# Performance work log

Measured on AMD Instinct MI355X. Metric: run time of the kernel, lower is better.

## Reference

```python
import jax, jax.numpy as jnp
import numpy as np


def sine_encode_2d(pos, d):
    # pos: (..., 2) normalized relative positions in [-1, 1]; output (..., d)
    # standard sinusoidal encoding per coordinate, d/2 dims each (sin/cos pairs)
    d_half = d // 2
    n_freq = d_half // 2
    freqs = jnp.exp(-jnp.log(jnp.float32(10000.0)) * jnp.arange(n_freq, dtype=jnp.float32) / n_freq)
    parts = []
    for i in range(2):
        ang = pos[..., i:i + 1] * freqs  # (..., n_freq)
        parts.append(jnp.sin(ang))
        parts.append(jnp.cos(ang))
    return jnp.concatenate(parts, axis=-1)


def rpe_bias(W_rpe, t_q, f_q, t_k, f_k, N_t, N_f, d_rpe):
    dt_norm = jnp.arange(-(N_t - 1), N_t, dtype=jnp.float32) / max(N_t - 1, 1)
    df_norm = jnp.arange(-(N_f - 1), N_f, dtype=jnp.float32) / max(N_f - 1, 1)
    DT, DF = jnp.meshgrid(dt_norm, df_norm, indexing='ij')       # (2Nt-1, 2Nf-1)
    rel = jnp.stack([DT, DF], axis=-1)                            # (2Nt-1, 2Nf-1, 2)
    enc = sine_encode_2d(rel, d_rpe)                              # (2Nt-1, 2Nf-1, d_rpe)
    table = enc @ W_rpe.T                                         # (2Nt-1, 2Nf-1, h)
    n_df = 2 * N_f - 1
    flat = table.reshape(-1, table.shape[-1])                     # ((2Nt-1)*(2Nf-1), h)
    dt_idx = t_q[:, None] - t_k[None, :] + (N_t - 1)              # (Nq, Nk)
    df_idx = f_q[:, None] - f_k[None, :] + (N_f - 1)
    flat_idx = jnp.clip(dt_idx * n_df + df_idx, 0, flat.shape[0] - 1)
    bias = flat[flat_idx]                                         # (Nq, Nk, h)
    return jnp.transpose(bias, (2, 0, 1))                         # (h, Nq, Nk)


def setup_inputs() -> dict:
    key = jax.random.key(0)
    ks = jax.random.split(key, 12)
    B, N_t, N_f, d_model, n_heads, d_rpe = 8, 14, 72, 256, 8, 32
    N = N_t * N_f
    s = 1.0 / np.sqrt(d_model)
    return {
        'q_tokens': jax.random.normal(ks[0], (B, N, d_model), jnp.float32),
        'k_tokens': jax.random.normal(ks[1], (B, N, d_model), jnp.float32),
        'v_tokens': jax.random.normal(ks[2], (B, N, d_model), jnp.float32),
        't_q': jax.random.randint(ks[3], (N,), 0, N_t),
        'f_q': jax.random.randint(ks[4], (N,), 0, N_f),
        't_k': jax.random.randint(ks[5], (N,), 0, N_t),
        'f_k': jax.random.randint(ks[6], (N,), 0, N_f),
        'N_t': N_t,
        'N_f': N_f,
        'W_q': jax.random.normal(ks[7], (d_model, d_model), jnp.float32) * s,
        'W_k': jax.random.normal(ks[8], (d_model, d_model), jnp.float32) * s,
        'W_v': jax.random.normal(ks[9], (d_model, d_model), jnp.float32) * s,
        'W_o': jax.random.normal(ks[10], (d_model, d_model), jnp.float32) * s,
        'W_rpe': jax.random.normal(ks[11], (n_heads, d_rpe), jnp.float32) * (1.0 / np.sqrt(d_rpe)),
    }


def reference(q_tokens, k_tokens, v_tokens, t_q, f_q, t_k, f_k, N_t, N_f,
              W_q, W_k, W_v, W_o, W_rpe):
    B, N_q, d_model = q_tokens.shape
    N_k = k_tokens.shape[1]
    h = W_rpe.shape[0]
    d_rpe = W_rpe.shape[1]
    dk = d_model // h
    scale = jnp.float32(np.sqrt(dk))
    Q = (q_tokens @ W_q.T).reshape(B, N_q, h, dk)
    K = (k_tokens @ W_k.T).reshape(B, N_k, h, dk)
    V = (v_tokens @ W_v.T).reshape(B, N_k, h, dk)
    scores = jnp.einsum('bqhd,bkhd->bhqk', Q, K) / scale          # (B, h, Nq, Nk)
    bias = rpe_bias(W_rpe, t_q, f_q, t_k, f_k, N_t, N_f, d_rpe)   # (h, Nq, Nk)
    attn = jax.nn.softmax(scores + bias[None], axis=-1)
    out = jnp.einsum('bhqk,bkhd->bqhd', attn, V).reshape(B, N_q, d_model)
    return out @ W_o.T
```

## Files before the change

### kernel.cpp

```cpp
#include <hip/hip_runtime.h>

#define B_    8
#define N_    1008
#define D_    256
#define H_    8
#define DK_   32
#define DA_   64
#define L2E_  1.4426950408889634f

typedef _Float16 half8_t __attribute__((ext_vector_type(8)));
typedef _Float16 half4_t __attribute__((ext_vector_type(4)));
typedef float    f32x4   __attribute__((ext_vector_type(4)));

#if defined(__has_builtin)
#if __has_builtin(__builtin_amdgcn_exp2f)
#define EXP2(x) __builtin_amdgcn_exp2f(x)
#else
#define EXP2(x) exp2f(x)
#endif
#else
#define EXP2(x) exp2f(x)
#endif

__global__ __launch_bounds__(256, 4) void qkv_prep(
    const float* __restrict__ q_tok, const float* __restrict__ k_tok,
    const float* __restrict__ v_tok,
    const int* __restrict__ t_q, const int* __restrict__ f_q,
    const int* __restrict__ t_k, const int* __restrict__ f_k,
    const float* __restrict__ Wq, const float* __restrict__ Wk,
    const float* __restrict__ Wv, const float* __restrict__ W_rpe,
    _Float16* __restrict__ Qq, _Float16* __restrict__ Kq,
    _Float16* __restrict__ Uq, _Float16* __restrict__ Vr,
    _Float16* __restrict__ Vt)
{
    __shared__ __align__(16) _Float16 fw[8 * 4 * 64 * 8];
    const int tid = threadIdx.x;
    const int lane = tid & 63, w = tid >> 6, quad = lane >> 4, l15 = lane & 15;
    const int id = blockIdx.x;

    if (id < 756) {
        const int mtile = id / 12, rem = id % 12, z = rem >> 2, ntile = rem & 3;
        const int m0 = mtile * 128, n0 = ntile * 64;
        const float* A = (z == 0) ? q_tok : (z == 1) ? k_tok : v_tok;
        const float* W = (z == 0) ? Wq : (z == 1) ? Wk : Wv;

        const float* Ar0 = &A[(size_t)(m0 + w * 16 + l15) * D_];
        const float* Ar1 = Ar0 + (size_t)64 * D_;
        float4 a00 = *(const float4*)&Ar0[quad * 8];
        float4 a01 = *(const float4*)&Ar0[quad * 8 + 4];
        float4 a10 = *(const float4*)&Ar1[quad * 8];
        float4 a11 = *(const float4*)&Ar1[quad * 8 + 4];

#pragma unroll
        for (int p = 0; p < 8; p++) {
            int g = p * 256 + tid;
            int ch = g >> 8, rem2 = g & 255, nt = rem2 >> 6, L = rem2 & 63;
            const float* src = &W[(size_t)(n0 + nt * 16 + (L & 15)) * D_ + ch * 32 + ((L >> 4) & 3) * 8];
            float4 w0 = *(const float4*)src;
            float4 w1 = *(const float4*)(src + 4);
            half8_t hv = {(_Float16)w0.x, (_Float16)w0.y, (_Float16)w0.z, (_Float16)w0.w,
                          (_Float16)w1.x, (_Float16)w1.y, (_Float16)w1.z, (_Float16)w1.w};
            *(half8_t*)&fw[g * 8] = hv;
        }
        __syncthreads();

        f32x4 acc[2][4] = {};
#pragma unroll
        for (int ch = 0; ch < 8; ch++) {
            half8_t af0 = {(_Float16)a00.x, (_Float16)a00.y, (_Float16)a00.z, (_Float16)a00.w,
                           (_Float16)a01.x, (_Float16)a01.y, (_Float16)a01.z, (_Float16)a01.w};
            half8_t af1 = {(_Float16)a10.x, (_Float16)a10.y, (_Float16)a10.z, (_Float16)a10.w,
                           (_Float16)a11.x, (_Float16)a11.y, (_Float16)a11.z, (_Float16)a11.w};
            if (ch < 7) {
                a00 = *(const float4*)&Ar0[(ch + 1) * 32 + quad * 8];
                a01 = *(const float4*)&Ar0[(ch + 1) * 32 + quad * 8 + 4];
                a10 = *(const float4*)&Ar1[(ch + 1) * 32 + quad * 8];
                a11 = *(const float4*)&Ar1[(ch + 1) * 32 + quad * 8 + 4];
            }
#pragma unroll
            for (int nt = 0; nt < 4; nt++) {
                half8_t bf = *(const half8_t*)&fw[((ch * 4 + nt) * 64 + lane) * 8];
                acc[0][nt] = __builtin_amdgcn_mfma_f32_16x16x32_f16(af0, bf, acc[0][nt], 0, 0, 0);
                acc[1][nt] = __builtin_amdgcn_mfma_f32_16x16x32_f16(af1, bf, acc[1][nt], 0, 0, 0);
            }
        }
        const float scale = (z == 0) ? 0.17677669529663687f * L2E_ : 1.0f;
#pragma unroll
        for (int mt = 0; mt < 2; mt++) {
            int mbase = m0 + mt * 64 + w * 16 + quad * 4;
            int b = mbase / N_;
            int q = mbase - b * N_;
            if (z < 2) {
                _Float16* o = (z == 0) ? Qq : Kq;
#pragma unroll
                for (int nt = 0; nt < 4; nt++) {
                    int n = n0 + nt * 16 + l15;
                    int hh = n >> 5, d = n & 31;
                    _Float16* dst = &o[(((size_t)(b * 8 + hh)) * N_ + q) * DK_ + d];
#pragma unroll
                    for (int r = 0; r < 4; r++)
                        dst[(size_t)r * DK_] = (_Float16)(acc[mt][nt][r] * scale);
                }
            } else {
#pragma unroll
                for (int nt = 0; nt < 4; nt++) {
                    int n = n0 + nt * 16 + l15;
                    int hh = n >> 5, d = n & 31;
                    half4_t o = {(_Float16)acc[mt][nt][0], (_Float16)acc[mt][nt][1],
                                 (_Float16)acc[mt][nt][2], (_Float16)acc[mt][nt][3]};
                    *(half4_t*)&Vt[(((size_t)(b * 8 + hh)) * DK_ + d) * N_ + q] = o;
                }
            }
        }
    } else {
        const float FR[8] = {1.f, 0.31622776601683794f, 0.1f, 0.03162277660168379f,
                             0.01f, 0.0031622776601683794f, 0.001f, 0.00031622776601683794f};
        int gid = (id - 756) * 256 + tid;
        if (gid < N_ * H_) {
            int q = gid >> 3, h = gid & 7;
            float tq = (float)t_q[q] * (1.f / 13.f);
            float fq = (float)f_q[q] * (1.f / 71.f);
            const float* Wh = W_rpe + h * 32;
            half8_t u0, u1, u2, u3;
#pragma unroll
            for (int i = 0; i < 8; i++) {
                float sa = __sinf(tq * FR[i]), ca = __cosf(tq * FR[i]);
                float sb = __sinf(fq * FR[i]), cb = __cosf(fq * FR[i]);
                u0[i] = (_Float16)(L2E_ * (Wh[i] * sa + Wh[8 + i] * ca));
                u1[i] = (_Float16)(L2E_ * (Wh[8 + i] * sa - Wh[i] * ca));
                u2[i] = (_Float16)(L2E_ * (Wh[16 + i] * sb + Wh[24 + i] * cb));
                u3[i] = (_Float16)(L2E_ * (Wh[24 + i] * sb - Wh[16 + i] * cb));
            }
            _Float16* dst = &Uq[((size_t)h * N_ + q) * DK_];
            *(half8_t*)(dst + 0) = u0;  *(half8_t*)(dst + 8) = u1;
            *(half8_t*)(dst + 16) = u2; *(half8_t*)(dst + 24) = u3;
        } else if (gid < N_ * H_ + N_) {
            int k = gid - N_ * H_;
            float tk = (float)t_k[k] * (1.f / 13.f);
            float fk = (float)f_k[k] * (1.f / 71.f);
            half8_t v0, v1, v2, v3;
#pragma unroll
            for (int i = 0; i < 8; i++) {
                v0[i] = (_Float16)__cosf(tk * FR[i]);
                v1[i] = (_Float16)__sinf(tk * FR[i]);
                v2[i] = (_Float16)__cosf(fk * FR[i]);
                v3[i] = (_Float16)__sinf(fk * FR[i]);
            }
            _Float16* dst = &Vr[(size_t)k * DK_];
            *(half8_t*)(dst + 0) = v0;  *(half8_t*)(dst + 8) = v1;
            *(half8_t*)(dst + 16) = v2; *(half8_t*)(dst + 24) = v3;
        }
    }
}

__global__ __launch_bounds__(256, 4) void attn(const _Float16* __restrict__ Qq,
    const _Float16* __restrict__ Kq, const _Float16* __restrict__ Uq,
    const _Float16* __restrict__ Vr, const _Float16* __restrict__ Vt,
    _Float16* __restrict__ AO)
{
    __shared__ __align__(16) _Float16 fkl[2][4096];
    __shared__ __align__(16) _Float16 fvl[2][2048];
    __shared__ __align__(16) _Float16 pl[4][16][72];

    const int tid = threadIdx.x;
    const int lane = tid & 63, w = tid >> 6, quad = lane >> 4, l15 = lane & 15;
    const int bh = blockIdx.x, q0 = blockIdx.y * 64;
    const int b = bh >> 3, hh = bh & 7;
    const _Float16* Kb = Kq + (size_t)bh * N_ * DK_;
    const _Float16* Vb = Vt + (size_t)bh * DK_ * N_;

    const int s_l15 = tid & 15, s_quad = (tid >> 4) & 3;
    const int s_mt = tid >> 6;
    const int s_c = tid >> 7;
    const int s_mt2 = (tid >> 6) & 1;

    const int qg = q0 + w * 16 + l15;
    const int qc = qg < N_ ? qg : N_ - 1;
    half8_t qf0 = *(const half8_t*)&Qq[((size_t)bh * N_ + qc) * DK_ + quad * 8];
    half8_t qf1 = *(const half8_t*)&Uq[((size_t)hh * N_ + qc) * DK_ + quad * 8];

    float m_run = -1e30f, l_run = 0.f;
    f32x4 O[2] = {};

    {
        int krow = s_mt * 16 + s_l15;
        *(half8_t*)&fkl[0][((s_mt * 2 + 0) * 64 + lane) * 8] =
            *(const half8_t*)&Kb[(size_t)krow * DK_ + s_quad * 8];
        *(half8_t*)&fkl[0][((s_mt * 2 + 1) * 64 + lane) * 8] =
            *(const half8_t*)&Vr[(size_t)krow * DK_ + s_quad * 8];
        int vrow = s_mt2 * 16 + s_l15;
        int vcol = s_c * 32 + s_quad * 8;
        *(half8_t*)&fvl[0][tid * 8] = *(const half8_t*)&Vb[(size_t)vrow * N_ + vcol];
    }
    __syncthreads();

    for (int kt = 0; kt < 16; kt++) {
        const int cb = kt & 1;
        half8_t nk0, nk1, nv;
        if (kt < 15) {
            int k0n = (kt + 1) * 64;
            int krow = k0n + s_mt * 16 + s_l15;
            if (krow > N_ - 1) krow = N_ - 1;
            nk0 = *(const half8_t*)&Kb[(size_t)krow * DK_ + s_quad * 8];
            nk1 = *(const half8_t*)&Vr[(size_t)krow * DK_ + s_quad * 8];
            int vrow = s_mt2 * 16 + s_l15;
            int vcol = k0n + s_c * 32 + s_quad * 8;
            if (vcol > N_ - 8) vcol = N_ - 8;
            nv = *(const half8_t*)&Vb[(size_t)vrow * N_ + vcol];
        }
        f32x4 S[4];
        __builtin_amdgcn_s_setprio(1);
#pragma unroll
        for (int mt = 0; mt < 4; mt++) {
            half8_t kf0 = *(const half8_t*)&fkl[cb][((mt * 2 + 0) * 64 + lane) * 8];
            half8_t kf1 = *(const half8_t*)&fkl[cb][((mt * 2 + 1) * 64 + lane) * 8];
            f32x4 zz = {0.f, 0.f, 0.f, 0.f};
            zz = __builtin_amdgcn_mfma_f32_16x16x32_f16(kf0, qf0, zz, 0, 0, 0);
            S[mt] = __builtin_amdgcn_mfma_f32_16x16x32_f16(kf1, qf1, zz, 0, 0, 0);
        }
        __builtin_amdgcn_s_setprio(0);
        if (kt == 15)
            S[3] = (f32x4){-1e30f, -1e30f, -1e30f, -1e30f};
        float x0 = fmaxf(fmaxf(S[0][0], S[0][1]), fmaxf(S[0][2], S[0][3]));
        float x1 = fmaxf(fmaxf(S[1][0], S[1][1]), fmaxf(S[1][2], S[1][3]));
        float x2 = fmaxf(fmaxf(S[2][0], S[2][1]), fmaxf(S[2][2], S[2][3]));
        float x3 = fmaxf(fmaxf(S[3][0], S[3][1]), fmaxf(S[3][2], S[3][3]));
        float tmax = fmaxf(fmaxf(x0, x1), fmaxf(x2, x3));
        tmax = fmaxf(tmax, __shfl_xor(tmax, 16, 64));
        tmax = fmaxf(tmax, __shfl_xor(tmax, 32, 64));
        float mnew = fmaxf(m_run, tmax);
        float alpha = EXP2(m_run - mnew);
        m_run = mnew;
        float tsum = 0.f;
#pragma unroll
        for (int mt = 0; mt < 4; mt++) {
            float p0 = EXP2(S[mt][0] - mnew), p1 = EXP2(S[mt][1] - mnew);
            float p2 = EXP2(S[mt][2] - mnew), p3 = EXP2(S[mt][3] - mnew);
            tsum += (p0 + p1) + (p2 + p3);
            half4_t ph = {(_Float16)p0, (_Float16)p1, (_Float16)p2, (_Float16)p3};
            *(half4_t*)&pl[w][l15][mt * 16 + quad * 4] = ph;
        }
        tsum += __shfl_xor(tsum, 16, 64);
        tsum += __shfl_xor(tsum, 32, 64);
        l_run = l_run * alpha + tsum;
        O[0] = O[0] * alpha;
        O[1] = O[1] * alpha;
        __builtin_amdgcn_s_setprio(1);
#pragma unroll
        for (int c = 0; c < 2; c++) {
            half8_t pf = *(const half8_t*)&pl[w][l15][c * 32 + quad * 8];
            half8_t vfa = *(const half8_t*)&fvl[cb][((c * 2 + 0) * 64 + lane) * 8];
            half8_t vfb = *(const half8_t*)&fvl[cb][((c * 2 + 1) * 64 + lane) * 8];
            O[0] = __builtin_amdgcn_mfma_f32_16x16x32_f16(vfa, pf, O[0], 0, 0, 0);
            O[1] = __builtin_amdgcn_mfma_f32_16x16x32_f16(vfb, pf, O[1], 0, 0, 0);
        }
        __builtin_amdgcn_s_setprio(0);
        if (kt < 15) {
            *(half8_t*)&fkl[cb ^ 1][((s_mt * 2 + 0) * 64 + lane) * 8] = nk0;
            *(half8_t*)&fkl[cb ^ 1][((s_mt * 2 + 1) * 64 + lane) * 8] = nk1;
            *(half8_t*)&fvl[cb ^ 1][tid * 8] = nv;
        }
        __syncthreads();
    }
    if (qg < N_) {
        float inv = 1.f / l_run;
#pragma unroll
        for (int mt2 = 0; mt2 < 2; mt2++) {
            half4_t o = {(_Float16)(O[mt2][0] * inv), (_Float16)(O[mt2][1] * inv),
                         (_Float16)(O[mt2][2] * inv), (_Float16)(O[mt2][3] * inv)};
            *(half4_t*)&AO[((size_t)b * N_ + qg) * D_ + hh * DK_ + mt2 * 16 + quad * 4] = o;
        }
    }
}

__global__ __launch_bounds__(256, 4) void out_gemm(const _Float16* __restrict__ A,
    const float* __restrict__ W, float* __restrict__ out)
{
    __shared__ __align__(16) _Float16 fw[8 * 4 * 64 * 8];
    const int tid = threadIdx.x;
    const int lane = tid & 63, w = tid >> 6, quad = lane >> 4, l15 = lane & 15;
    const int id = blockIdx.x;
    const int m0 = (id >> 2) * 64, n0 = (id & 3) * 64;

    const _Float16* Ar = &A[(size_t)(m0 + w * 16 + l15) * D_];
    half8_t af = *(const half8_t*)&Ar[quad * 8];

#pragma unroll
    for (int p = 0; p < 8; p++) {
        int g = p * 256 + tid;
        int ch = g >> 8, rem2 = g & 255, nt = rem2 >> 6, L = rem2 & 63;
        const float* src = &W[(size_t)(n0 + nt * 16 + (L & 15)) * D_ + ch * 32 + ((L >> 4) & 3) * 8];
        float4 w0 = *(const float4*)src;
        float4 w1 = *(const float4*)(src + 4);
        half8_t hv = {(_Float16)w0.x, (_Float16)w0.y, (_Float16)w0.z, (_Float16)w0.w,
                      (_Float16)w1.x, (_Float16)w1.y, (_Float16)w1.z, (_Float16)w1.w};
        *(half8_t*)&fw[g * 8] = hv;
    }
    __syncthreads();

    f32x4 acc[4] = {};
#pragma unroll
    for (int ch = 0; ch < 8; ch++) {
        half8_t c0 = af;
        if (ch < 7) af = *(const half8_t*)&Ar[(ch + 1) * 32 + quad * 8];
#pragma unroll
        for (int nt = 0; nt < 4; nt++) {
            half8_t bf = *(const half8_t*)&fw[((ch * 4 + nt) * 64 + lane) * 8];
            acc[nt] = __builtin_amdgcn_mfma_f32_16x16x32_f16(c0, bf, acc[nt], 0, 0, 0);
        }
    }
    const int mbase = m0 + w * 16 + quad * 4;
#pragma unroll
    for (int nt = 0; nt < 4; nt++) {
        int n = n0 + nt * 16 + l15;
#pragma unroll
        for (int r = 0; r < 4; r++)
            out[(size_t)(mbase + r) * D_ + n] = acc[nt][r];
    }
}

extern "C" void kernel_launch(void* const* d_in, const int* in_sizes, int n_in,
                              void* d_out, int out_size, void* d_ws, size_t ws_size,
                              hipStream_t stream)
{
    const float* q_tokens = (const float*)d_in[0];
    const float* k_tokens = (const float*)d_in[1];
    const float* v_tokens = (const float*)d_in[2];
    const int*   t_q      = (const int*)d_in[3];
    const int*   f_q      = (const int*)d_in[4];
    const int*   t_k      = (const int*)d_in[5];
    const int*   f_k      = (const int*)d_in[6];
    const float* W_q   = (const float*)d_in[9];
    const float* W_k   = (const float*)d_in[10];
    const float* W_v   = (const float*)d_in[11];
    const float* W_o   = (const float*)d_in[12];
    const float* W_rpe = (const float*)d_in[13];

    _Float16* ws = (_Float16*)d_ws;
    _Float16* Qq = ws;
    _Float16* Kq = Qq + (size_t)64 * N_ * DK_;
    _Float16* Uq = Kq + (size_t)64 * N_ * DK_;
    _Float16* Vr = Uq + (size_t)H_ * N_ * DK_;
    _Float16* Vt = Vr + (size_t)N_ * DK_;
    _Float16* AO = Vt + (size_t)64 * DK_ * N_;

    qkv_prep<<<dim3(792), 256, 0, stream>>>(q_tokens, k_tokens, v_tokens,
                                            t_q, f_q, t_k, f_k,
                                            W_q, W_k, W_v, W_rpe,
                                            Qq, Kq, Uq, Vr, Vt);
    attn<<<dim3(64, 16), 256, 0, stream>>>(Qq, Kq, Uq, Vr, Vt, AO);
    out_gemm<<<dim3(504), 256, 0, stream>>>(AO, W_o, (float*)d_out);
}
```

Measured before the change: 145.8 us.

## Process two query tiles per attention block and skip small softmax rescales

Each attention workgroup now handles 128 queries instead of 64, with every wave carrying two 16-row query fragments. Each K/V tile staged in shared memory is therefore reused twice, and half as many blocks reload K and V. The online-softmax rescale is also skipped when the new tile max exceeds the running max by at most 8 (in log2 units) across the wavefront, which removes exp and multiply work but allows unnormalized probabilities up to 256 before fp16 conversion. Register pressure roughly doubles (launch bounds lowered to 2), and the grid shrinks to 512 blocks, which may reduce occupancy on the many-CU device.

```diff
diff --git a/kernel.cpp b/kernel.cpp
--- a/kernel.cpp
+++ b/kernel.cpp
@@ -153,18 +153,18 @@
     }
 }
 
-__global__ __launch_bounds__(256, 4) void attn(const _Float16* __restrict__ Qq,
+__global__ __launch_bounds__(256, 2) void attn(const _Float16* __restrict__ Qq,
     const _Float16* __restrict__ Kq, const _Float16* __restrict__ Uq,
     const _Float16* __restrict__ Vr, const _Float16* __restrict__ Vt,
     _Float16* __restrict__ AO)
 {
     __shared__ __align__(16) _Float16 fkl[2][4096];
     __shared__ __align__(16) _Float16 fvl[2][2048];
-    __shared__ __align__(16) _Float16 pl[4][16][72];
+    __shared__ __align__(16) _Float16 pl[4][2][16][72];
 
     const int tid = threadIdx.x;
     const int lane = tid & 63, w = tid >> 6, quad = lane >> 4, l15 = lane & 15;
-    const int bh = blockIdx.x, q0 = blockIdx.y * 64;
+    const int bh = blockIdx.x, q0 = blockIdx.y * 128;
     const int b = bh >> 3, hh = bh & 7;
     const _Float16* Kb = Kq + (size_t)bh * N_ * DK_;
     const _Float16* Vb = Vt + (size_t)bh * DK_ * N_;
@@ -174,13 +174,16 @@
     const int s_c = tid >> 7;
     const int s_mt2 = (tid >> 6) & 1;
 
-    const int qg = q0 + w * 16 + l15;
-    const int qc = qg < N_ ? qg : N_ - 1;
-    half8_t qf0 = *(const half8_t*)&Qq[((size_t)bh * N_ + qc) * DK_ + quad * 8];
-    half8_t qf1 = *(const half8_t*)&Uq[((size_t)hh * N_ + qc) * DK_ + quad * 8];
-
-    float m_run = -1e30f, l_run = 0.f;
-    f32x4 O[2] = {};
+    const int qgA = q0 + w * 16 + l15, qgB = qgA + 64;
+    const int qcA = qgA < N_ ? qgA : N_ - 1;
+    const int qcB = qgB < N_ ? qgB : N_ - 1;
+    half8_t qf0A = *(const half8_t*)&Qq[((size_t)bh * N_ + qcA) * DK_ + quad * 8];
+    half8_t qf1A = *(const half8_t*)&Uq[((size_t)hh * N_ + qcA) * DK_ + quad * 8];
+    half8_t qf0B = *(const half8_t*)&Qq[((size_t)bh * N_ + qcB) * DK_ + quad * 8];
+    half8_t qf1B = *(const half8_t*)&Uq[((size_t)hh * N_ + qcB) * DK_ + quad * 8];
+
+    float mA = -1e30f, lA = 0.f, mB = -1e30f, lB = 0.f;
+    f32x4 OA[2] = {}, OB[2] = {};
 
     {
         int krow = s_mt * 16 + s_l15;
@@ -208,51 +211,89 @@
             if (vcol > N_ - 8) vcol = N_ - 8;
             nv = *(const half8_t*)&Vb[(size_t)vrow * N_ + vcol];
         }
-        f32x4 S[4];
+        f32x4 SA[4], SB[4];
         __builtin_amdgcn_s_setprio(1);
 #pragma unroll
         for (int mt = 0; mt < 4; mt++) {
             half8_t kf0 = *(const half8_t*)&fkl[cb][((mt * 2 + 0) * 64 + lane) * 8];
             half8_t kf1 = *(const half8_t*)&fkl[cb][((mt * 2 + 1) * 64 + lane) * 8];
-            f32x4 zz = {0.f, 0.f, 0.f, 0.f};
-            zz = __builtin_amdgcn_mfma_f32_16x16x32_f16(kf0, qf0, zz, 0, 0, 0);
-            S[mt] = __builtin_amdgcn_mfma_f32_16x16x32_f16(kf1, qf1, zz, 0, 0, 0);
+            f32x4 za = {0.f, 0.f, 0.f, 0.f};
+            za = __builtin_amdgcn_mfma_f32_16x16x32_f16(kf0, qf0A, za, 0, 0, 0);
+            SA[mt] = __builtin_amdgcn_mfma_f32_16x16x32_f16(kf1, qf1A, za, 0, 0, 0);
+            f32x4 zb = {0.f, 0.f, 0.f, 0.f};
+            zb = __builtin_amdgcn_mfma_f32_16x16x32_f16(kf0, qf0B, zb, 0, 0, 0);
+            SB[mt] = __builtin_amdgcn_mfma_f32_16x16x32_f16(kf1, qf1B, zb, 0, 0, 0);
         }
         __builtin_amdgcn_s_setprio(0);
-        if (kt == 15)
-            S[3] = (f32x4){-1e30f, -1e30f, -1e30f, -1e30f};
-        float x0 = fmaxf(fmaxf(S[0][0], S[0][1]), fmaxf(S[0][2], S[0][3]));
-        float x1 = fmaxf(fmaxf(S[1][0], S[1][1]), fmaxf(S[1][2], S[1][3]));
-        float x2 = fmaxf(fmaxf(S[2][0], S[2][1]), fmaxf(S[2][2], S[2][3]));
-        float x3 = fmaxf(fmaxf(S[3][0], S[3][1]), fmaxf(S[3][2], S[3][3]));
-        float tmax = fmaxf(fmaxf(x0, x1), fmaxf(x2, x3));
-        tmax = fmaxf(tmax, __shfl_xor(tmax, 16, 64));
-        tmax = fmaxf(tmax, __shfl_xor(tmax, 32, 64));
-        float mnew = fmaxf(m_run, tmax);
-        float alpha = EXP2(m_run - mnew);
-        m_run = mnew;
-        float tsum = 0.f;
-#pragma unroll
-        for (int mt = 0; mt < 4; mt++) {
-            float p0 = EXP2(S[mt][0] - mnew), p1 = EXP2(S[mt][1] - mnew);
-            float p2 = EXP2(S[mt][2] - mnew), p3 = EXP2(S[mt][3] - mnew);
-            tsum += (p0 + p1) + (p2 + p3);
-            half4_t ph = {(_Float16)p0, (_Float16)p1, (_Float16)p2, (_Float16)p3};
-            *(half4_t*)&pl[w][l15][mt * 16 + quad * 4] = ph;
-        }
-        tsum += __shfl_xor(tsum, 16, 64);
-        tsum += __shfl_xor(tsum, 32, 64);
-        l_run = l_run * alpha + tsum;
-        O[0] = O[0] * alpha;
-        O[1] = O[1] * alpha;
+        if (kt == 15) {
+            SA[3] = (f32x4){-1e30f, -1e30f, -1e30f, -1e30f};
+            SB[3] = (f32x4){-1e30f, -1e30f, -1e30f, -1e30f};
+        }
+        {
+            float x0 = fmaxf(fmaxf(SA[0][0], SA[0][1]), fmaxf(SA[0][2], SA[0][3]));
+            float x1 = fmaxf(fmaxf(SA[1][0], SA[1][1]), fmaxf(SA[1][2], SA[1][3]));
+            float x2 = fmaxf(fmaxf(SA[2][0], SA[2][1]), fmaxf(SA[2][2], SA[2][3]));
+            float x3 = fmaxf(fmaxf(SA[3][0], SA[3][1]), fmaxf(SA[3][2], SA[3][3]));
+            float tmax = fmaxf(fmaxf(x0, x1), fmaxf(x2, x3));
+            tmax = fmaxf(tmax, __shfl_xor(tmax, 16, 64));
+            tmax = fmaxf(tmax, __shfl_xor(tmax, 32, 64));
+            if (!__all(tmax - mA <= 8.f)) {
+                float mn = fmaxf(mA, tmax);
+                float alpha = EXP2(mA - mn);
+                mA = mn;  lA *= alpha;
+                OA[0] = OA[0] * alpha;  OA[1] = OA[1] * alpha;
+            }
+            float tsum = 0.f;
+#pragma unroll
+            for (int mt = 0; mt < 4; mt++) {
+                float p0 = EXP2(SA[mt][0] - mA), p1 = EXP2(SA[mt][1] - mA);
+                float p2 = EXP2(SA[mt][2] - mA), p3 = EXP2(SA[mt][3] - mA);
+                tsum += (p0 + p1) + (p2 + p3);
+                half4_t ph = {(_Float16)p0, (_Float16)p1, (_Float16)p2, (_Float16)p3};
+                *(half4_t*)&pl[w][0][l15][mt * 16 + quad * 4] = ph;
+            }
+            tsum += __shfl_xor(tsum, 16, 64);
+            tsum += __shfl_xor(tsum, 32, 64);
+            lA += tsum;
+        }
+        {
+            float x0 = fmaxf(fmaxf(SB[0][0], SB[0][1]), fmaxf(SB[0][2], SB[0][3]));
+            float x1 = fmaxf(fmaxf(SB[1][0], SB[1][1]), fmaxf(SB[1][2], SB[1][3]));
+            float x2 = fmaxf(fmaxf(SB[2][0], SB[2][1]), fmaxf(SB[2][2], SB[2][3]));
+            float x3 = fmaxf(fmaxf(SB[3][0], SB[3][1]), fmaxf(SB[3][2], SB[3][3]));
+            float tmax = fmaxf(fmaxf(x0, x1), fmaxf(x2, x3));
+            tmax = fmaxf(tmax, __shfl_xor(tmax, 16, 64));
+            tmax = fmaxf(tmax, __shfl_xor(tmax, 32, 64));
+            if (!__all(tmax - mB <= 8.f)) {
+                float mn = fmaxf(mB, tmax);
+                float alpha = EXP2(mB - mn);
+                mB = mn;  lB *= alpha;
+                OB[0] = OB[0] * alpha;  OB[1] = OB[1] * alpha;
+            }
+            float tsum = 0.f;
+#pragma unroll
+            for (int mt = 0; mt < 4; mt++) {
+                float p0 = EXP2(SB[mt][0] - mB), p1 = EXP2(SB[mt][1] - mB);
+                float p2 = EXP2(SB[mt][2] - mB), p3 = EXP2(SB[mt][3] - mB);
+                tsum += (p0 + p1) + (p2 + p3);
+                half4_t ph = {(_Float16)p0, (_Float16)p1, (_Float16)p2, (_Float16)p3};
+                *(half4_t*)&pl[w][1][l15][mt * 16 + quad * 4] = ph;
+            }
+            tsum += __shfl_xor(tsum, 16, 64);
+            tsum += __shfl_xor(tsum, 32, 64);
+            lB += tsum;
+        }
         __builtin_amdgcn_s_setprio(1);
 #pragma unroll
         for (int c = 0; c < 2; c++) {
-            half8_t pf = *(const half8_t*)&pl[w][l15][c * 32 + quad * 8];
             half8_t vfa = *(const half8_t*)&fvl[cb][((c * 2 + 0) * 64 + lane) * 8];
             half8_t vfb = *(const half8_t*)&fvl[cb][((c * 2 + 1) * 64 + lane) * 8];
-            O[0] = __builtin_amdgcn_mfma_f32_16x16x32_f16(vfa, pf, O[0], 0, 0, 0);
-            O[1] = __builtin_amdgcn_mfma_f32_16x16x32_f16(vfb, pf, O[1], 0, 0, 0);
+            half8_t pfA = *(const half8_t*)&pl[w][0][l15][c * 32 + quad * 8];
+            half8_t pfB = *(const half8_t*)&pl[w][1][l15][c * 32 + quad * 8];
+            OA[0] = __builtin_amdgcn_mfma_f32_16x16x32_f16(vfa, pfA, OA[0], 0, 0, 0);
+            OA[1] = __builtin_amdgcn_mfma_f32_16x16x32_f16(vfb, pfA, OA[1], 0, 0, 0);
+            OB[0] = __builtin_amdgcn_mfma_f32_16x16x32_f16(vfa, pfB, OB[0], 0, 0, 0);
+            OB[1] = __builtin_amdgcn_mfma_f32_16x16x32_f16(vfb, pfB, OB[1], 0, 0, 0);
         }
         __builtin_amdgcn_s_setprio(0);
         if (kt < 15) {
@@ -262,13 +303,22 @@
         }
         __syncthreads();
     }
-    if (qg < N_) {
-        float inv = 1.f / l_run;
+    if (qgA < N_) {
+        float inv = 1.f / lA;
 #pragma unroll
         for (int mt2 = 0; mt2 < 2; mt2++) {
-            half4_t o = {(_Float16)(O[mt2][0] * inv), (_Float16)(O[mt2][1] * inv),
-                         (_Float16)(O[mt2][2] * inv), (_Float16)(O[mt2][3] * inv)};
-            *(half4_t*)&AO[((size_t)b * N_ + qg) * D_ + hh * DK_ + mt2 * 16 + quad * 4] = o;
+            half4_t o = {(_Float16)(OA[mt2][0] * inv), (_Float16)(OA[mt2][1] * inv),
+                         (_Float16)(OA[mt2][2] * inv), (_Float16)(OA[mt2][3] * inv)};
+            *(half4_t*)&AO[((size_t)b * N_ + qgA) * D_ + hh * DK_ + mt2 * 16 + quad * 4] = o;
+        }
+    }
+    if (qgB < N_) {
+        float inv = 1.f / lB;
+#pragma unroll
+        for (int mt2 = 0; mt2 < 2; mt2++) {
+            half4_t o = {(_Float16)(OB[mt2][0] * inv), (_Float16)(OB[mt2][1] * inv),
+                         (_Float16)(OB[mt2][2] * inv), (_Float16)(OB[mt2][3] * inv)};
+            *(half4_t*)&AO[((size_t)b * N_ + qgB) * D_ + hh * DK_ + mt2 * 16 + quad * 4] = o;
         }
     }
 }
@@ -348,6 +398,6 @@
                                             t_q, f_q, t_k, f_k,
                                             W_q, W_k, W_v, W_rpe,
                                             Qq, Kq, Uq, Vr, Vt);
-    attn<<<dim3(64, 16), 256, 0, stream>>>(Qq, Kq, Uq, Vr, Vt, AO);
+    attn<<<dim3(64, 8), 256, 0, stream>>>(Qq, Kq, Uq, Vr, Vt, AO);
     out_gemm<<<dim3(504), 256, 0, stream>>>(AO, W_o, (float*)d_out);
 }
```

After: 147.6 us. Within noise of the previous version (+1.2%).
